# Kernel tuning notes

Measured on AMD Instinct MI355X. Metric: run time of the kernel, lower is better.

The kernel has to match this reference:

```python
import jax, jax.numpy as jnp
import numpy as np
import math

B, L, D, H = 2, 2048, 1024, 16
HD = D // H

def setup_inputs() -> dict:
    key = jax.random.key(0)
    ks = jax.random.split(key, 8)
    s = 1.0 / math.sqrt(D)
    # causal additive mask: 0 on/below diagonal, -inf above
    causal = jnp.where(jnp.tril(jnp.ones((L, L), dtype=bool)), 0.0, -jnp.inf)
    causal = causal[None, None].astype(jnp.float32)  # [1,1,L,L]
    return {
        "Q": jax.random.normal(ks[0], (B, L, D), jnp.float32),
        "K": jax.random.normal(ks[1], (B, L, D), jnp.float32),
        "V": jax.random.normal(ks[2], (B, L, D), jnp.float32),
        "attn_mask": causal,
        "padding_mask": jnp.zeros((B, L), dtype=bool),
        "wq": jax.random.normal(ks[3], (D, D), jnp.float32) * s,
        "wk": jax.random.normal(ks[4], (D, D), jnp.float32) * s,
        "wv": jax.random.normal(ks[5], (D, D), jnp.float32) * s,
        "wout": jax.random.normal(ks[6], (D, D), jnp.float32) * s,
    }

def reference(Q, K, V, attn_mask, padding_mask, wq, wk, wv, wout):
    b, l, _ = Q.shape
    # projections (torch Linear: x @ W.T); weights sampled as [out,in]-like square
    def proj(x, w):
        return (x @ w.T).reshape(b, l, H, HD).transpose(0, 2, 1, 3)  # [B,H,L,hd]
    q = proj(Q, wq)
    k = proj(K, wk)
    v = proj(V, wv)
    scores = jnp.einsum("bhqd,bhkd->bhqk", q, k) / math.sqrt(HD)
    scores = scores + attn_mask
    scores = jnp.where(padding_mask[:, None, None, :], -jnp.inf, scores)
    weights = jax.nn.softmax(scores, axis=-1)
    ctx = jnp.einsum("bhqk,bhkd->bhqd", weights, v)
    ctx = ctx.transpose(0, 2, 1, 3).reshape(b, l, D)
    return ctx @ wout.T
```

## Files before the change

### kernel.cpp

```cpp
#include <hip/hip_runtime.h>
#include <stdint.h>
#include <stddef.h>

typedef __bf16 bf16_t;
typedef bf16_t bf16x4 __attribute__((ext_vector_type(4)));
typedef bf16_t bf16x8 __attribute__((ext_vector_type(8)));
typedef float f32x4 __attribute__((ext_vector_type(4)));

#define MFMA_BF16(A_, B_, C_) __builtin_amdgcn_mfma_f32_16x16x32_bf16(A_, B_, C_, 0, 0, 0)

static constexpr int Lseq = 2048;
static constexpr int Dmod = 1024;
static constexpr int Hn   = 16;
static constexpr int HDim = 64;
static constexpr size_t M1 = 1u << 20;

__device__ __forceinline__ int swz(int row, int chunk) {
  return row * 64 + ((chunk ^ (row & 7)) << 3);
}

__device__ __forceinline__ void async_ld16(const bf16_t* g, bf16_t* l) {
  __builtin_amdgcn_global_load_lds(
      (const __attribute__((address_space(1))) void*)g,
      (__attribute__((address_space(3))) void*)l, 16, 0, 0);
}

__global__ __launch_bounds__(256) void cvt_kernel(
    const float* __restrict__ Q, const float* __restrict__ K,
    const float* __restrict__ V, const float* __restrict__ wq,
    const float* __restrict__ wk, const float* __restrict__ wv,
    const float* __restrict__ wout, bf16_t* __restrict__ wsb)
{
  const int s = blockIdx.z;
  const float* __restrict__ src;
  if      (s < 4)   src = Q    + (size_t)s * M1;
  else if (s < 8)   src = K    + (size_t)(s - 4) * M1;
  else if (s < 12)  src = V    + (size_t)(s - 8) * M1;
  else if (s == 12) src = wq;
  else if (s == 13) src = wk;
  else if (s == 14) src = wv;
  else              src = wout;
  bf16_t* __restrict__ dst = wsb + (size_t)s * M1;

  const int t = blockIdx.x * 256 + threadIdx.x;
#pragma unroll
  for (int j = 0; j < 4; ++j) {
    const int i4 = t + j * 65536;
    float4 v4 = ((const float4*)src)[i4];
    bf16x4 b4;
    b4[0] = (bf16_t)v4.x; b4[1] = (bf16_t)v4.y;
    b4[2] = (bf16_t)v4.z; b4[3] = (bf16_t)v4.w;
    ((bf16x4*)dst)[i4] = b4;
  }
}

__global__ __launch_bounds__(256) void proj_kernel(
    const bf16_t* __restrict__ Qbf, const bf16_t* __restrict__ Kbf,
    const bf16_t* __restrict__ Vbf, const bf16_t* __restrict__ wqb,
    const bf16_t* __restrict__ wkb, const bf16_t* __restrict__ wvb,
    bf16_t* __restrict__ qo, bf16_t* __restrict__ ko, bf16_t* __restrict__ vo)
{
  const int z = blockIdx.z;
  const bf16_t* __restrict__ A  = (z == 0) ? Qbf : (z == 1) ? Kbf : Vbf;
  const bf16_t* __restrict__ Bw = (z == 0) ? wqb : (z == 1) ? wkb : wvb;
  bf16_t* __restrict__ dst      = (z == 0) ? qo  : (z == 1) ? ko  : vo;

  __shared__ __align__(16) bf16_t As[128 * 64];
  __shared__ __align__(16) bf16_t Bs[128 * 64];

  const int tid  = threadIdx.x;
  const int wave = tid >> 6;
  const int lane = tid & 63;
  const int quad = lane >> 4;
  const int l16  = lane & 15;
  const int wm   = (wave & 1) * 64;
  const int wn   = (wave >> 1) * 64;
  const int m0   = blockIdx.y * 128;
  const int n0   = blockIdx.x * 128;

  const int srow8  = lane >> 3;
  const int schunk = (lane & 7) ^ srow8;

  f32x4 acc[4][4];
#pragma unroll
  for (int i = 0; i < 4; ++i)
#pragma unroll
    for (int j = 0; j < 4; ++j)
#pragma unroll
      for (int e = 0; e < 4; ++e) acc[i][j][e] = 0.0f;

  for (int kt = 0; kt < 16; ++kt) {
    const int k0 = kt * 64;
    __syncthreads();
#pragma unroll
    for (int i = 0; i < 4; ++i) {
      const int rb = wave * 32 + i * 8;
      async_ld16(&A [(size_t)(m0 + rb + srow8) * Dmod + k0 + schunk * 8], &As[rb * 64]);
      async_ld16(&Bw[(size_t)(n0 + rb + srow8) * Dmod + k0 + schunk * 8], &Bs[rb * 64]);
    }
    __syncthreads();

    bf16x8 af[4][2], bfr[4][2];
#pragma unroll
    for (int mt = 0; mt < 4; ++mt) {
      const int row = wm + mt * 16 + l16;
      af[mt][0] = *(const bf16x8*)&As[swz(row, quad)];
      af[mt][1] = *(const bf16x8*)&As[swz(row, quad + 4)];
    }
#pragma unroll
    for (int nt = 0; nt < 4; ++nt) {
      const int row = wn + nt * 16 + l16;
      bfr[nt][0] = *(const bf16x8*)&Bs[swz(row, quad)];
      bfr[nt][1] = *(const bf16x8*)&Bs[swz(row, quad + 4)];
    }
#pragma unroll
    for (int mt = 0; mt < 4; ++mt)
#pragma unroll
      for (int nt = 0; nt < 4; ++nt) {
        acc[mt][nt] = MFMA_BF16(af[mt][0], bfr[nt][0], acc[mt][nt]);
        acc[mt][nt] = MFMA_BF16(af[mt][1], bfr[nt][1], acc[mt][nt]);
      }
  }

#pragma unroll
  for (int mt = 0; mt < 4; ++mt) {
    const int grb = m0 + wm + mt * 16 + quad * 4;
    const int bb  = grb >> 11;
    const int lb  = grb & 2047;
#pragma unroll
    for (int nt = 0; nt < 4; ++nt) {
      const int gc = n0 + wn + nt * 16 + l16;
      const int h  = gc >> 6;
      const int hd = gc & 63;
      if (z == 2) {
        bf16x4 pk;
#pragma unroll
        for (int r = 0; r < 4; ++r) pk[r] = (bf16_t)acc[mt][nt][r];
        *(bf16x4*)&dst[(((size_t)(bb * Hn + h) * HDim + hd) << 11) + lb] = pk;
      } else {
#pragma unroll
        for (int r = 0; r < 4; ++r)
          dst[(((size_t)(bb * Hn + h) * Lseq + lb + r) << 6) + hd] = (bf16_t)acc[mt][nt][r];
      }
    }
  }
}

__global__ __launch_bounds__(256) void attn_kernel(
    const bf16_t* __restrict__ q, const bf16_t* __restrict__ k,
    const bf16_t* __restrict__ v, bf16_t* __restrict__ ctx)
{
  const int px = blockIdx.x;
  const int bh = blockIdx.y;
  const int bb = bh >> 4;
  const int h  = bh & 15;

  const int tid  = threadIdx.x;
  const int wave = tid >> 6;
  const int lane = tid & 63;
  const int quad = lane >> 4;
  const int l16  = lane & 15;

  __shared__ __align__(16) bf16_t Ks[2][64 * 64];
  __shared__ __align__(16) bf16_t Vs[2][64 * 64];
  __shared__ __align__(16) bf16_t Ps[4][16][72];

  const bf16_t* __restrict__ qb = q + (size_t)bh * (Lseq * HDim);
  const bf16_t* __restrict__ kb = k + (size_t)bh * (Lseq * HDim);
  const bf16_t* __restrict__ vb = v + (size_t)bh * (HDim * Lseq);

  const int srow8  = lane >> 3;
  const int schunk = (lane & 7) ^ srow8;

  bf16x8 ones;
#pragma unroll
  for (int i = 0; i < 8; ++i) ones[i] = (bf16_t)1.0f;

  for (int half = 0; half < 2; ++half) {
    const int qt = half ? (31 - px) : px;
    const int q0 = qt * 64;
    const int qrow = q0 + wave * 16 + l16;

    bf16x8 qf0 = *(const bf16x8*)&qb[(size_t)qrow * HDim + quad * 8];
    bf16x8 qf1 = *(const bf16x8*)&qb[(size_t)qrow * HDim + 32 + quad * 8];

    f32x4 o[4];
    f32x4 lacc;
#pragma unroll
    for (int e = 0; e < 4; ++e) lacc[e] = 0.0f;
#pragma unroll
    for (int nt = 0; nt < 4; ++nt)
#pragma unroll
      for (int e = 0; e < 4; ++e) o[nt][e] = 0.0f;

    __syncthreads();
#pragma unroll
    for (int i = 0; i < 2; ++i) {
      const int rb = wave * 16 + i * 8;
      const int r  = rb + srow8;
      async_ld16(&kb[(size_t)r * HDim + schunk * 8], &Ks[0][rb * 64]);
      async_ld16(&vb[(size_t)r * Lseq + schunk * 8], &Vs[0][rb * 64]);
    }

    for (int jt = 0; jt <= qt; ++jt) {
      const int cur = jt & 1;
      __syncthreads();

      if (jt < qt) {
        const int j1 = (jt + 1) * 64;
#pragma unroll
        for (int i = 0; i < 2; ++i) {
          const int rb = wave * 16 + i * 8;
          const int r  = rb + srow8;
          async_ld16(&kb[(size_t)(j1 + r) * HDim + schunk * 8], &Ks[cur ^ 1][rb * 64]);
          async_ld16(&vb[(size_t)r * Lseq + j1 + schunk * 8], &Vs[cur ^ 1][rb * 64]);
        }
      }

      f32x4 s[4];
#pragma unroll
      for (int nt = 0; nt < 4; ++nt) {
#pragma unroll
        for (int e = 0; e < 4; ++e) s[nt][e] = 0.0f;
        const int krow = nt * 16 + l16;
        bf16x8 kf0 = *(const bf16x8*)&Ks[cur][swz(krow, quad)];
        bf16x8 kf1 = *(const bf16x8*)&Ks[cur][swz(krow, quad + 4)];
        s[nt] = MFMA_BF16(kf0, qf0, s[nt]);
        s[nt] = MFMA_BF16(kf1, qf1, s[nt]);
      }

      const bool diag = (jt == qt);
#pragma unroll
      for (int nt = 0; nt < 4; ++nt) {
        bf16x4 pk;
#pragma unroll
        for (int r = 0; r < 4; ++r) {
          float val = s[nt][r] * 0.18033688f;
          if (diag && (nt * 16 + quad * 4 + r > wave * 16 + l16)) val = -1e30f;
          pk[r] = (bf16_t)__builtin_amdgcn_exp2f(val);
        }
        *(bf16x4*)&Ps[wave][l16][nt * 16 + quad * 4] = pk;
      }

      bf16x8 pf0 = *(const bf16x8*)&Ps[wave][l16][quad * 8];
      bf16x8 pf1 = *(const bf16x8*)&Ps[wave][l16][32 + quad * 8];

      lacc = MFMA_BF16(pf0, ones, lacc);
      lacc = MFMA_BF16(pf1, ones, lacc);

#pragma unroll
      for (int nt = 0; nt < 4; ++nt) {
        const int vrow = nt * 16 + l16;
        bf16x8 vf0 = *(const bf16x8*)&Vs[cur][swz(vrow, quad)];
        bf16x8 vf1 = *(const bf16x8*)&Vs[cur][swz(vrow, quad + 4)];
        o[nt] = MFMA_BF16(pf0, vf0, o[nt]);
        o[nt] = MFMA_BF16(pf1, vf1, o[nt]);
      }
    }

    float inv[4];
#pragma unroll
    for (int r = 0; r < 4; ++r) inv[r] = 1.0f / lacc[r];
#pragma unroll
    for (int nt = 0; nt < 4; ++nt)
#pragma unroll
      for (int r = 0; r < 4; ++r) {
        const int gq = q0 + wave * 16 + quad * 4 + r;
        ctx[(size_t)(bb * Lseq + gq) * Dmod + h * HDim + nt * 16 + l16] =
            (bf16_t)(o[nt][r] * inv[r]);
      }
  }
}

__global__ __launch_bounds__(256) void out_kernel(
    const bf16_t* __restrict__ Actx, const bf16_t* __restrict__ Bwout,
    float* __restrict__ out)
{
  __shared__ __align__(16) bf16_t As[128 * 64];
  __shared__ __align__(16) bf16_t Bs[128 * 64];

  const int tid  = threadIdx.x;
  const int wave = tid >> 6;
  const int lane = tid & 63;
  const int quad = lane >> 4;
  const int l16  = lane & 15;
  const int wm   = (wave & 1) * 64;
  const int wn   = (wave >> 1) * 64;
  const int m0   = blockIdx.y * 128;
  const int n0   = blockIdx.x * 128;

  const int srow8  = lane >> 3;
  const int schunk = (lane & 7) ^ srow8;

  f32x4 acc[4][4];
#pragma unroll
  for (int i = 0; i < 4; ++i)
#pragma unroll
    for (int j = 0; j < 4; ++j)
#pragma unroll
      for (int e = 0; e < 4; ++e) acc[i][j][e] = 0.0f;

  for (int kt = 0; kt < 16; ++kt) {
    const int k0 = kt * 64;
    __syncthreads();
#pragma unroll
    for (int i = 0; i < 4; ++i) {
      const int rb = wave * 32 + i * 8;
      async_ld16(&Actx [(size_t)(m0 + rb + srow8) * Dmod + k0 + schunk * 8], &As[rb * 64]);
      async_ld16(&Bwout[(size_t)(n0 + rb + srow8) * Dmod + k0 + schunk * 8], &Bs[rb * 64]);
    }
    __syncthreads();

    bf16x8 af[4][2], bfr[4][2];
#pragma unroll
    for (int mt = 0; mt < 4; ++mt) {
      const int row = wm + mt * 16 + l16;
      af[mt][0] = *(const bf16x8*)&As[swz(row, quad)];
      af[mt][1] = *(const bf16x8*)&As[swz(row, quad + 4)];
    }
#pragma unroll
    for (int nt = 0; nt < 4; ++nt) {
      const int row = wn + nt * 16 + l16;
      bfr[nt][0] = *(const bf16x8*)&Bs[swz(row, quad)];
      bfr[nt][1] = *(const bf16x8*)&Bs[swz(row, quad + 4)];
    }
#pragma unroll
    for (int mt = 0; mt < 4; ++mt)
#pragma unroll
      for (int nt = 0; nt < 4; ++nt) {
        acc[mt][nt] = MFMA_BF16(af[mt][0], bfr[nt][0], acc[mt][nt]);
        acc[mt][nt] = MFMA_BF16(af[mt][1], bfr[nt][1], acc[mt][nt]);
      }
  }

#pragma unroll
  for (int mt = 0; mt < 4; ++mt) {
    const int grb = m0 + wm + mt * 16 + quad * 4;
#pragma unroll
    for (int nt = 0; nt < 4; ++nt) {
      const int gc = n0 + wn + nt * 16 + l16;
#pragma unroll
      for (int r = 0; r < 4; ++r)
        out[(size_t)(grb + r) * Dmod + gc] = acc[mt][nt][r];
    }
  }
}

extern "C" void kernel_launch(void* const* d_in, const int* in_sizes, int n_in,
                              void* d_out, int out_size, void* d_ws, size_t ws_size,
                              hipStream_t stream) {
  (void)in_sizes; (void)n_in; (void)out_size; (void)ws_size;
  const float* Q    = (const float*)d_in[0];
  const float* K    = (const float*)d_in[1];
  const float* V    = (const float*)d_in[2];
  const float* wq   = (const float*)d_in[5];
  const float* wk   = (const float*)d_in[6];
  const float* wv   = (const float*)d_in[7];
  const float* wout = (const float*)d_in[8];
  float* out = (float*)d_out;

  bf16_t* wsb = (bf16_t*)d_ws;
  bf16_t* Qbf   = wsb;
  bf16_t* Kbf   = wsb + 4 * M1;
  bf16_t* Vbf   = wsb + 8 * M1;
  bf16_t* wqb   = wsb + 12 * M1;
  bf16_t* wkb   = wsb + 13 * M1;
  bf16_t* wvb   = wsb + 14 * M1;
  bf16_t* woutb = wsb + 15 * M1;
  bf16_t* qp    = wsb + 16 * M1;
  bf16_t* kp    = wsb + 20 * M1;
  bf16_t* vp    = wsb + 24 * M1;
  bf16_t* cws   = wsb;

  cvt_kernel<<<dim3(256, 1, 16), 256, 0, stream>>>(Q, K, V, wq, wk, wv, wout, wsb);
  proj_kernel<<<dim3(8, 32, 3), 256, 0, stream>>>(Qbf, Kbf, Vbf, wqb, wkb, wvb, qp, kp, vp);
  attn_kernel<<<dim3(16, 32), 256, 0, stream>>>(qp, kp, vp, cws);
  out_kernel<<<dim3(8, 32), 256, 0, stream>>>(cws, woutb, out);
}
```

Baseline: 233.1 us.

## Retile GEMMs to 128x64, widen attention to 128-query blocks, vectorize conversion

The projection and output GEMMs move from 128x128 to 128x64 tiles, doubling block count to improve occupancy and CU fill. The attention kernel now uses 512 threads covering 128 query rows per block and shares each K/V tile across eight waves. Diagonal masking becomes per-wave based on absolute positions. The conversion kernel processes eight floats per thread with twice as many blocks. The trade-off is fewer launched attention blocks (256) and more redundant A-tile loads in the GEMMs.

```diff
diff --git a/kernel.cpp b/kernel.cpp
--- a/kernel.cpp
+++ b/kernel.cpp
@@ -42,16 +42,13 @@
   else              src = wout;
   bf16_t* __restrict__ dst = wsb + (size_t)s * M1;
 
-  const int t = blockIdx.x * 256 + threadIdx.x;
-#pragma unroll
-  for (int j = 0; j < 4; ++j) {
-    const int i4 = t + j * 65536;
-    float4 v4 = ((const float4*)src)[i4];
-    bf16x4 b4;
-    b4[0] = (bf16_t)v4.x; b4[1] = (bf16_t)v4.y;
-    b4[2] = (bf16_t)v4.z; b4[3] = (bf16_t)v4.w;
-    ((bf16x4*)dst)[i4] = b4;
-  }
+  const int idx = blockIdx.x * 256 + threadIdx.x;
+  float4 a = ((const float4*)src)[idx * 2];
+  float4 b = ((const float4*)src)[idx * 2 + 1];
+  bf16x8 o;
+  o[0] = (bf16_t)a.x; o[1] = (bf16_t)a.y; o[2] = (bf16_t)a.z; o[3] = (bf16_t)a.w;
+  o[4] = (bf16_t)b.x; o[5] = (bf16_t)b.y; o[6] = (bf16_t)b.z; o[7] = (bf16_t)b.w;
+  ((bf16x8*)dst)[idx] = o;
 }
 
 __global__ __launch_bounds__(256) void proj_kernel(
@@ -66,7 +63,7 @@
   bf16_t* __restrict__ dst      = (z == 0) ? qo  : (z == 1) ? ko  : vo;
 
   __shared__ __align__(16) bf16_t As[128 * 64];
-  __shared__ __align__(16) bf16_t Bs[128 * 64];
+  __shared__ __align__(16) bf16_t Bs[64 * 64];
 
   const int tid  = threadIdx.x;
   const int wave = tid >> 6;
@@ -74,18 +71,18 @@
   const int quad = lane >> 4;
   const int l16  = lane & 15;
   const int wm   = (wave & 1) * 64;
-  const int wn   = (wave >> 1) * 64;
+  const int wn   = (wave >> 1) * 32;
+  const int n0   = blockIdx.x * 64;
   const int m0   = blockIdx.y * 128;
-  const int n0   = blockIdx.x * 128;
 
   const int srow8  = lane >> 3;
   const int schunk = (lane & 7) ^ srow8;
 
-  f32x4 acc[4][4];
+  f32x4 acc[4][2];
 #pragma unroll
   for (int i = 0; i < 4; ++i)
 #pragma unroll
-    for (int j = 0; j < 4; ++j)
+    for (int j = 0; j < 2; ++j)
 #pragma unroll
       for (int e = 0; e < 4; ++e) acc[i][j][e] = 0.0f;
 
@@ -95,12 +92,16 @@
 #pragma unroll
     for (int i = 0; i < 4; ++i) {
       const int rb = wave * 32 + i * 8;
-      async_ld16(&A [(size_t)(m0 + rb + srow8) * Dmod + k0 + schunk * 8], &As[rb * 64]);
+      async_ld16(&A[(size_t)(m0 + rb + srow8) * Dmod + k0 + schunk * 8], &As[rb * 64]);
+    }
+#pragma unroll
+    for (int i = 0; i < 2; ++i) {
+      const int rb = wave * 16 + i * 8;
       async_ld16(&Bw[(size_t)(n0 + rb + srow8) * Dmod + k0 + schunk * 8], &Bs[rb * 64]);
     }
     __syncthreads();
 
-    bf16x8 af[4][2], bfr[4][2];
+    bf16x8 af[4][2], bfr[2][2];
 #pragma unroll
     for (int mt = 0; mt < 4; ++mt) {
       const int row = wm + mt * 16 + l16;
@@ -108,7 +109,7 @@
       af[mt][1] = *(const bf16x8*)&As[swz(row, quad + 4)];
     }
 #pragma unroll
-    for (int nt = 0; nt < 4; ++nt) {
+    for (int nt = 0; nt < 2; ++nt) {
       const int row = wn + nt * 16 + l16;
       bfr[nt][0] = *(const bf16x8*)&Bs[swz(row, quad)];
       bfr[nt][1] = *(const bf16x8*)&Bs[swz(row, quad + 4)];
@@ -116,7 +117,7 @@
 #pragma unroll
     for (int mt = 0; mt < 4; ++mt)
 #pragma unroll
-      for (int nt = 0; nt < 4; ++nt) {
+      for (int nt = 0; nt < 2; ++nt) {
         acc[mt][nt] = MFMA_BF16(af[mt][0], bfr[nt][0], acc[mt][nt]);
         acc[mt][nt] = MFMA_BF16(af[mt][1], bfr[nt][1], acc[mt][nt]);
       }
@@ -128,7 +129,7 @@
     const int bb  = grb >> 11;
     const int lb  = grb & 2047;
 #pragma unroll
-    for (int nt = 0; nt < 4; ++nt) {
+    for (int nt = 0; nt < 2; ++nt) {
       const int gc = n0 + wn + nt * 16 + l16;
       const int h  = gc >> 6;
       const int hd = gc & 63;
@@ -146,7 +147,7 @@
   }
 }
 
-__global__ __launch_bounds__(256) void attn_kernel(
+__global__ __launch_bounds__(512) void attn_kernel(
     const bf16_t* __restrict__ q, const bf16_t* __restrict__ k,
     const bf16_t* __restrict__ v, bf16_t* __restrict__ ctx)
 {
@@ -163,7 +164,7 @@
 
   __shared__ __align__(16) bf16_t Ks[2][64 * 64];
   __shared__ __align__(16) bf16_t Vs[2][64 * 64];
-  __shared__ __align__(16) bf16_t Ps[4][16][72];
+  __shared__ __align__(16) bf16_t Ps[8][16][72];
 
   const bf16_t* __restrict__ qb = q + (size_t)bh * (Lseq * HDim);
   const bf16_t* __restrict__ kb = k + (size_t)bh * (Lseq * HDim);
@@ -171,14 +172,15 @@
 
   const int srow8  = lane >> 3;
   const int schunk = (lane & 7) ^ srow8;
+  const int rb     = wave * 8;
 
   bf16x8 ones;
 #pragma unroll
   for (int i = 0; i < 8; ++i) ones[i] = (bf16_t)1.0f;
 
   for (int half = 0; half < 2; ++half) {
-    const int qt = half ? (31 - px) : px;
-    const int q0 = qt * 64;
+    const int qblk = half ? (15 - px) : px;
+    const int q0   = qblk * 128;
     const int qrow = q0 + wave * 16 + l16;
 
     bf16x8 qf0 = *(const bf16x8*)&qb[(size_t)qrow * HDim + quad * 8];
@@ -194,29 +196,22 @@
       for (int e = 0; e < 4; ++e) o[nt][e] = 0.0f;
 
     __syncthreads();
-#pragma unroll
-    for (int i = 0; i < 2; ++i) {
-      const int rb = wave * 16 + i * 8;
-      const int r  = rb + srow8;
-      async_ld16(&kb[(size_t)r * HDim + schunk * 8], &Ks[0][rb * 64]);
-      async_ld16(&vb[(size_t)r * Lseq + schunk * 8], &Vs[0][rb * 64]);
-    }
-
-    for (int jt = 0; jt <= qt; ++jt) {
+    async_ld16(&kb[(size_t)(rb + srow8) * HDim + schunk * 8], &Ks[0][rb * 64]);
+    async_ld16(&vb[(size_t)(rb + srow8) * Lseq + schunk * 8], &Vs[0][rb * 64]);
+
+    const int njt = 2 * qblk + 2;
+    const int diag_start = 2 * qblk + (wave >> 2);
+    for (int jt = 0; jt < njt; ++jt) {
       const int cur = jt & 1;
       __syncthreads();
 
-      if (jt < qt) {
+      if (jt + 1 < njt) {
         const int j1 = (jt + 1) * 64;
-#pragma unroll
-        for (int i = 0; i < 2; ++i) {
-          const int rb = wave * 16 + i * 8;
-          const int r  = rb + srow8;
-          async_ld16(&kb[(size_t)(j1 + r) * HDim + schunk * 8], &Ks[cur ^ 1][rb * 64]);
-          async_ld16(&vb[(size_t)r * Lseq + j1 + schunk * 8], &Vs[cur ^ 1][rb * 64]);
-        }
-      }
-
+        async_ld16(&kb[(size_t)(j1 + rb + srow8) * HDim + schunk * 8], &Ks[cur ^ 1][rb * 64]);
+        async_ld16(&vb[(size_t)(rb + srow8) * Lseq + j1 + schunk * 8], &Vs[cur ^ 1][rb * 64]);
+      }
+
+      const int j0 = jt * 64;
       f32x4 s[4];
 #pragma unroll
       for (int nt = 0; nt < 4; ++nt) {
@@ -229,14 +224,14 @@
         s[nt] = MFMA_BF16(kf1, qf1, s[nt]);
       }
 
-      const bool diag = (jt == qt);
+      const bool need_mask = (jt >= diag_start);
 #pragma unroll
       for (int nt = 0; nt < 4; ++nt) {
         bf16x4 pk;
 #pragma unroll
         for (int r = 0; r < 4; ++r) {
           float val = s[nt][r] * 0.18033688f;
-          if (diag && (nt * 16 + quad * 4 + r > wave * 16 + l16)) val = -1e30f;
+          if (need_mask && (j0 + nt * 16 + quad * 4 + r > qrow)) val = -1e30f;
           pk[r] = (bf16_t)__builtin_amdgcn_exp2f(val);
         }
         *(bf16x4*)&Ps[wave][l16][nt * 16 + quad * 4] = pk;
@@ -277,7 +272,7 @@
     float* __restrict__ out)
 {
   __shared__ __align__(16) bf16_t As[128 * 64];
-  __shared__ __align__(16) bf16_t Bs[128 * 64];
+  __shared__ __align__(16) bf16_t Bs[64 * 64];
 
   const int tid  = threadIdx.x;
   const int wave = tid >> 6;
@@ -285,18 +280,18 @@
   const int quad = lane >> 4;
   const int l16  = lane & 15;
   const int wm   = (wave & 1) * 64;
-  const int wn   = (wave >> 1) * 64;
+  const int wn   = (wave >> 1) * 32;
+  const int n0   = blockIdx.x * 64;
   const int m0   = blockIdx.y * 128;
-  const int n0   = blockIdx.x * 128;
 
   const int srow8  = lane >> 3;
   const int schunk = (lane & 7) ^ srow8;
 
-  f32x4 acc[4][4];
+  f32x4 acc[4][2];
 #pragma unroll
   for (int i = 0; i < 4; ++i)
 #pragma unroll
-    for (int j = 0; j < 4; ++j)
+    for (int j = 0; j < 2; ++j)
 #pragma unroll
       for (int e = 0; e < 4; ++e) acc[i][j][e] = 0.0f;
 
@@ -306,12 +301,16 @@
 #pragma unroll
     for (int i = 0; i < 4; ++i) {
       const int rb = wave * 32 + i * 8;
-      async_ld16(&Actx [(size_t)(m0 + rb + srow8) * Dmod + k0 + schunk * 8], &As[rb * 64]);
+      async_ld16(&Actx[(size_t)(m0 + rb + srow8) * Dmod + k0 + schunk * 8], &As[rb * 64]);
+    }
+#pragma unroll
+    for (int i = 0; i < 2; ++i) {
+      const int rb = wave * 16 + i * 8;
       async_ld16(&Bwout[(size_t)(n0 + rb + srow8) * Dmod + k0 + schunk * 8], &Bs[rb * 64]);
     }
     __syncthreads();
 
-    bf16x8 af[4][2], bfr[4][2];
+    bf16x8 af[4][2], bfr[2][2];
 #pragma unroll
     for (int mt = 0; mt < 4; ++mt) {
       const int row = wm + mt * 16 + l16;
@@ -319,7 +318,7 @@
       af[mt][1] = *(const bf16x8*)&As[swz(row, quad + 4)];
     }
 #pragma unroll
-    for (int nt = 0; nt < 4; ++nt) {
+    for (int nt = 0; nt < 2; ++nt) {
       const int row = wn + nt * 16 + l16;
       bfr[nt][0] = *(const bf16x8*)&Bs[swz(row, quad)];
       bfr[nt][1] = *(const bf16x8*)&Bs[swz(row, quad + 4)];
@@ -327,7 +326,7 @@
 #pragma unroll
     for (int mt = 0; mt < 4; ++mt)
 #pragma unroll
-      for (int nt = 0; nt < 4; ++nt) {
+      for (int nt = 0; nt < 2; ++nt) {
         acc[mt][nt] = MFMA_BF16(af[mt][0], bfr[nt][0], acc[mt][nt]);
         acc[mt][nt] = MFMA_BF16(af[mt][1], bfr[nt][1], acc[mt][nt]);
       }
@@ -337,7 +336,7 @@
   for (int mt = 0; mt < 4; ++mt) {
     const int grb = m0 + wm + mt * 16 + quad * 4;
 #pragma unroll
-    for (int nt = 0; nt < 4; ++nt) {
+    for (int nt = 0; nt < 2; ++nt) {
       const int gc = n0 + wn + nt * 16 + l16;
 #pragma unroll
       for (int r = 0; r < 4; ++r)
@@ -372,8 +371,8 @@
   bf16_t* vp    = wsb + 24 * M1;
   bf16_t* cws   = wsb;
 
-  cvt_kernel<<<dim3(256, 1, 16), 256, 0, stream>>>(Q, K, V, wq, wk, wv, wout, wsb);
-  proj_kernel<<<dim3(8, 32, 3), 256, 0, stream>>>(Qbf, Kbf, Vbf, wqb, wkb, wvb, qp, kp, vp);
-  attn_kernel<<<dim3(16, 32), 256, 0, stream>>>(qp, kp, vp, cws);
-  out_kernel<<<dim3(8, 32), 256, 0, stream>>>(cws, woutb, out);
-}
+  cvt_kernel<<<dim3(512, 1, 16), 256, 0, stream>>>(Q, K, V, wq, wk, wv, wout, wsb);
+  proj_kernel<<<dim3(16, 32, 3), 256, 0, stream>>>(Qbf, Kbf, Vbf, wqb, wkb, wvb, qp, kp, vp);
+  attn_kernel<<<dim3(8, 32), 512, 0, stream>>>(qp, kp, vp, cws);
+  out_kernel<<<dim3(16, 32), 256, 0, stream>>>(cws, woutb, out);
+}
```

New measurement: 225.5 us. -3.3%, faster.
